# Optimization experiments

Hardware: AMD Instinct MI355X
Metric: run time of the kernel (lower is better)

The kernel has to match this reference:

```python
import jax, jax.numpy as jnp
import numpy as np

N_F, N_R = 50000, 25000
E_FF, E_RR, E_RF = 400000, 200000, 400000
D_N, D_F, D_R, D_E = 128, 128, 128, 64  # node-in, furn-out, room-out, edge dims
W_SCALE = 0.02


def _w(key, shape):
    # positive weights keep attention-score segment sums away from zero
    return jnp.abs(jax.random.normal(key, shape, dtype=jnp.float32)) * W_SCALE


def _edges(key, n_src, n_dst, n_edges):
    k1, k2 = jax.random.split(key)
    src = jax.random.randint(k1, (n_edges,), 0, n_src)
    # guarantee every dst node has >=1 in-edge of this etype
    dst = jnp.concatenate([jnp.arange(n_dst),
                           jax.random.randint(k2, (n_edges - n_dst,), 0, n_dst)])
    return src, dst


def setup_inputs() -> dict:
    key = jax.random.key(0)
    ks = jax.random.split(key, 24)
    ff_src, ff_dst = _edges(ks[0], N_F, N_F, E_FF)
    rr_src, rr_dst = _edges(ks[1], N_R, N_R, E_RR)
    rf_src, rf_dst = _edges(ks[2], N_R, N_F, E_RF)
    return {
        'f_feat': jax.random.uniform(ks[3], (N_F, D_N), dtype=jnp.float32),
        'r_feat': jax.random.uniform(ks[4], (N_R, D_N), dtype=jnp.float32),
        'ff_efeat': jax.random.uniform(ks[5], (E_FF, D_E), dtype=jnp.float32),
        'rr_efeat': jax.random.uniform(ks[6], (E_RR, D_E), dtype=jnp.float32),
        'rf_efeat': jax.random.uniform(ks[7], (E_RF, D_E), dtype=jnp.float32),
        # node / edge projections (nn.Linear weight stored transposed: [in, out])
        'Wf': _w(ks[8], (D_N, D_F)), 'Wr': _w(ks[9], (D_N, D_R)),
        'We_ff': _w(ks[10], (D_E, D_E)), 'We_rr': _w(ks[11], (D_E, D_E)), 'We_rf': _w(ks[12], (D_E, D_E)),
        # attention vectors (Linear(cat_dim, 1) flattened)
        'a_ff': _w(ks[13], (2 * D_F + D_E,)),
        'a_rr': _w(ks[14], (2 * D_R + D_E,)),
        'a_rf': _w(ks[15], (D_R + D_F + D_E,)),
        # node-out -> edge-out converters
        'Wec_ff': _w(ks[16], (D_F, D_E)), 'Wec_rr': _w(ks[17], (D_R, D_E)), 'Wec_rf': _w(ks[18], (D_F, D_E)),
        # edge-out -> node-out converters
        'Wnc_ff': _w(ks[19], (D_E, D_F)), 'Wnc_rr': _w(ks[20], (D_E, D_R)), 'Wnc_rf': _w(ks[21], (D_E, D_F)),
        'ff_src': ff_src, 'ff_dst': ff_dst,
        'rr_src': rr_src, 'rr_dst': rr_dst,
        'rf_src': rf_src, 'rf_dst': rf_dst,
    }


def _lrelu(x):
    return jnp.where(x >= 0, x, 0.01 * x)


def reference(f_feat, r_feat, ff_efeat, rr_efeat, rf_efeat,
              Wf, Wr, We_ff, We_rr, We_rf, a_ff, a_rr, a_rf,
              Wec_ff, Wec_rr, Wec_rf, Wnc_ff, Wnc_rr, Wnc_rf,
              ff_src, ff_dst, rr_src, rr_dst, rf_src, rf_dst):
    n_f, n_r = f_feat.shape[0], r_feat.shape[0]
    seg = jax.ops.segment_sum

    # node / edge linear projections (computed once per node/edge, then gathered)
    hf = f_feat @ Wf            # [N_F, D_F]
    hr = r_feat @ Wr            # [N_R, D_R]
    eff = ff_efeat @ We_ff      # [E_FF, D_E]
    err = rr_efeat @ We_rr
    erf = rf_efeat @ We_rf

    # attention scores: leakyrelu(a . [W_src(src), W_dst(dst), W_e(e)])
    # split a into per-slot vectors so per-node dots are computed once
    s_ff = _lrelu(jnp.take(hf @ a_ff[:D_F], ff_src) + jnp.take(hf @ a_ff[D_F:2 * D_F], ff_dst) + eff @ a_ff[2 * D_F:])
    s_rr = _lrelu(jnp.take(hr @ a_rr[:D_R], rr_src) + jnp.take(hr @ a_rr[D_R:2 * D_R], rr_dst) + err @ a_rr[2 * D_R:])
    s_rf = _lrelu(jnp.take(hr @ a_rf[:D_R], rf_src) + jnp.take(hf @ a_rf[D_R:D_R + D_F], rf_dst) + erf @ a_rf[D_R + D_F:])

    # sum_scores accumulated at DST nodes (DGL update_all over ff, rf, rr)
    sum_f = seg(s_ff, ff_dst, num_segments=n_f) + seg(s_rf, rf_dst, num_segments=n_f)
    sum_r = seg(s_rr, rr_dst, num_segments=n_r)

    # normalization divides by the SRC node's sum_scores (as in the source)
    s_ff = s_ff / jnp.take(sum_f, ff_src)
    s_rf = s_rf / jnp.take(sum_r, rf_src)
    s_rr = s_rr / jnp.take(sum_r, rr_src)

    # edge feature update: score * (W_e_convert(W_node(dst)) + W_e(e))
    new_eff = s_ff[:, None] * (jnp.take(hf @ Wec_ff, ff_dst, axis=0) + eff)
    new_err = s_rr[:, None] * (jnp.take(hr @ Wec_rr, rr_dst, axis=0) + err)
    new_erf = s_rf[:, None] * (jnp.take(hf @ Wec_rf, rf_dst, axis=0) + erf)

    # node updates: scatter-sum of W_node_convert(edge) to dst; matmul after sum
    upd_f = seg(new_eff, ff_dst, num_segments=n_f) @ Wnc_ff + seg(new_erf, rf_dst, num_segments=n_f) @ Wnc_rf
    upd_r = seg(new_err, rr_dst, num_segments=n_r) @ Wnc_rr

    new_f = hf + _lrelu(upd_f)
    new_r = hr + _lrelu(upd_r)
    return new_f, new_r, new_eff, new_err, new_erf
```

## Files before the change

kernel.cpp:

```cpp
#include <hip/hip_runtime.h>
#include <hip/hip_bf16.h>

#define LRELU(x) ((x) >= 0.f ? (x) : 0.01f * (x))

static constexpr int N_F = 50000, N_R = 25000;
static constexpr int E_FF = 400000, E_RR = 200000, E_RF = 400000;

static constexpr size_t OFF_NF  = 0;
static constexpr size_t OFF_NR  = OFF_NF + (size_t)N_F * 128;
static constexpr size_t OFF_EFF = OFF_NR + (size_t)N_R * 128;
static constexpr size_t OFF_ERR = OFF_EFF + (size_t)E_FF * 64;
static constexpr size_t OFF_ERF = OFF_ERR + (size_t)E_RR * 64;

static constexpr size_t WS_HF      = 0;
static constexpr size_t WS_HR      = WS_HF + (size_t)N_F * 128;
static constexpr size_t WS_GFC_FF  = WS_HR + (size_t)N_R * 128;
static constexpr size_t WS_GFC_RF  = WS_GFC_FF + (size_t)N_F * 64;
static constexpr size_t WS_GRC_RR  = WS_GFC_RF + (size_t)N_F * 64;
static constexpr size_t WS_DF_FFS  = WS_GRC_RR + (size_t)N_R * 64;
static constexpr size_t WS_DF_FFD  = WS_DF_FFS + N_F;
static constexpr size_t WS_DF_RFD  = WS_DF_FFD + N_F;
static constexpr size_t WS_DR_RRS  = WS_DF_RFD + N_F;
static constexpr size_t WS_DR_RRD  = WS_DR_RRS + N_R;
static constexpr size_t WS_DR_RFS  = WS_DR_RRD + N_R;
static constexpr size_t WS_SFF     = WS_DR_RFS + N_R;
static constexpr size_t WS_SRR     = WS_SFF + E_FF;
static constexpr size_t WS_SRF     = WS_SRR + E_RR;
static constexpr size_t WS_WT      = WS_SRF + E_RF;
static constexpr size_t WS_SUMF    = WS_WT + 192;
static constexpr size_t WS_SUMR    = WS_SUMF + N_F;
static constexpr size_t WS_AGGF    = WS_SUMR + N_R;
static constexpr size_t WS_AGGRR   = WS_AGGF + (size_t)N_F * 128;
static constexpr size_t WS_END     = WS_AGGRR + (size_t)N_R * 64;
static constexpr size_t ZERO_OFF   = WS_SUMF;
static constexpr size_t ZERO_CNT   = WS_END - WS_SUMF;

__global__ void wtilde_k(const float* __restrict__ We_ff, const float* __restrict__ We_rr,
                         const float* __restrict__ We_rf, const float* __restrict__ a_ff,
                         const float* __restrict__ a_rr, const float* __restrict__ a_rf,
                         float* __restrict__ wt) {
  int t = threadIdx.x;
  if (t >= 192) return;
  int grp = t >> 6, k = t & 63;
  const float* W = (grp == 0) ? We_ff : (grp == 1) ? We_rr : We_rf;
  const float* a = (grp == 0) ? a_ff + 256 : (grp == 1) ? a_rr + 256 : a_rf + 256;
  float s = 0.f;
  #pragma unroll 8
  for (int j = 0; j < 64; ++j) s += W[k * 64 + j] * a[j];
  wt[t] = s;
}

__global__ __launch_bounds__(256)
void gemm_dot3_128(const float* __restrict__ A, const float* __restrict__ W,
                   const float* __restrict__ a0, const float* __restrict__ a1,
                   const float* __restrict__ a2, float* __restrict__ C,
                   float* __restrict__ d0, float* __restrict__ d1,
                   float* __restrict__ d2, int M) {
  constexpr int K = 128, N = 128, BM = 64, BK = 32;
  __shared__ float As[BM][BK + 1];
  __shared__ float Ws[BK][N];
  const int t = threadIdx.x;
  const int row0 = (int)blockIdx.x * BM;
  const int rg = t >> 4, cg = t & 15;
  const int r0 = rg * 4, c0 = cg * 4;

  float acc[4][8];
  #pragma unroll
  for (int i = 0; i < 4; ++i)
    #pragma unroll
    for (int j = 0; j < 8; ++j) acc[i][j] = 0.f;

  for (int kb = 0; kb < K; kb += BK) {
    #pragma unroll
    for (int u = 0; u < 2; ++u) {
      int id = t + u * 256;
      int ar = id >> 3, ac = (id & 7) * 4;
      float4 v = make_float4(0.f, 0.f, 0.f, 0.f);
      int grow = row0 + ar;
      if (grow < M) v = *reinterpret_cast<const float4*>(&A[(size_t)grow * K + kb + ac]);
      As[ar][ac] = v.x; As[ar][ac + 1] = v.y; As[ar][ac + 2] = v.z; As[ar][ac + 3] = v.w;
    }
    #pragma unroll
    for (int u = 0; u < 4; ++u) {
      int id = t + u * 256;
      int wr = id >> 5, wc = (id & 31) * 4;
      *reinterpret_cast<float4*>(&Ws[wr][wc]) =
          *reinterpret_cast<const float4*>(&W[(size_t)(kb + wr) * N + wc]);
    }
    __syncthreads();
    #pragma unroll
    for (int k = 0; k < BK; ++k) {
      float av[4] = {As[r0][k], As[r0 + 1][k], As[r0 + 2][k], As[r0 + 3][k]};
      float4 w0 = *reinterpret_cast<const float4*>(&Ws[k][c0]);
      float4 w1 = *reinterpret_cast<const float4*>(&Ws[k][c0 + 64]);
      #pragma unroll
      for (int i = 0; i < 4; ++i) {
        acc[i][0] += av[i] * w0.x; acc[i][1] += av[i] * w0.y;
        acc[i][2] += av[i] * w0.z; acc[i][3] += av[i] * w0.w;
        acc[i][4] += av[i] * w1.x; acc[i][5] += av[i] * w1.y;
        acc[i][6] += av[i] * w1.z; acc[i][7] += av[i] * w1.w;
      }
    }
    __syncthreads();
  }
  float4 a0l = *reinterpret_cast<const float4*>(&a0[c0]);
  float4 a0h = *reinterpret_cast<const float4*>(&a0[c0 + 64]);
  float4 a1l = *reinterpret_cast<const float4*>(&a1[c0]);
  float4 a1h = *reinterpret_cast<const float4*>(&a1[c0 + 64]);
  float4 a2l = *reinterpret_cast<const float4*>(&a2[c0]);
  float4 a2h = *reinterpret_cast<const float4*>(&a2[c0 + 64]);
  #pragma unroll
  for (int i = 0; i < 4; ++i) {
    int grow = row0 + r0 + i;
    if (grow < M) {
      *reinterpret_cast<float4*>(&C[(size_t)grow * N + c0]) =
          make_float4(acc[i][0], acc[i][1], acc[i][2], acc[i][3]);
      *reinterpret_cast<float4*>(&C[(size_t)grow * N + c0 + 64]) =
          make_float4(acc[i][4], acc[i][5], acc[i][6], acc[i][7]);
    }
    float p0 = acc[i][0] * a0l.x + acc[i][1] * a0l.y + acc[i][2] * a0l.z + acc[i][3] * a0l.w
             + acc[i][4] * a0h.x + acc[i][5] * a0h.y + acc[i][6] * a0h.z + acc[i][7] * a0h.w;
    float p1 = acc[i][0] * a1l.x + acc[i][1] * a1l.y + acc[i][2] * a1l.z + acc[i][3] * a1l.w
             + acc[i][4] * a1h.x + acc[i][5] * a1h.y + acc[i][6] * a1h.z + acc[i][7] * a1h.w;
    float p2 = acc[i][0] * a2l.x + acc[i][1] * a2l.y + acc[i][2] * a2l.z + acc[i][3] * a2l.w
             + acc[i][4] * a2h.x + acc[i][5] * a2h.y + acc[i][6] * a2h.z + acc[i][7] * a2h.w;
    #pragma unroll
    for (int off = 1; off < 16; off <<= 1) {
      p0 += __shfl_xor(p0, off);
      p1 += __shfl_xor(p1, off);
      p2 += __shfl_xor(p2, off);
    }
    if (cg == 0 && grow < M) { d0[grow] = p0; d1[grow] = p1; d2[grow] = p2; }
  }
}

__global__ __launch_bounds__(256)
void gemm_128x64(const float* __restrict__ A, const float* __restrict__ W,
                 float* __restrict__ C, int M) {
  constexpr int K = 128, N = 64, BM = 64, BK = 32;
  __shared__ float As[BM][BK + 1];
  __shared__ float Ws[BK][N];
  const int t = threadIdx.x;
  const int row0 = (int)blockIdx.x * BM;
  const int rg = t >> 4, cg = t & 15;
  const int r0 = rg * 4, c0 = cg * 4;
  float acc[4][4];
  #pragma unroll
  for (int i = 0; i < 4; ++i)
    #pragma unroll
    for (int j = 0; j < 4; ++j) acc[i][j] = 0.f;

  for (int kb = 0; kb < K; kb += BK) {
    #pragma unroll
    for (int u = 0; u < 2; ++u) {
      int id = t + u * 256;
      int ar = id >> 3, ac = (id & 7) * 4;
      float4 v = make_float4(0.f, 0.f, 0.f, 0.f);
      int grow = row0 + ar;
      if (grow < M) v = *reinterpret_cast<const float4*>(&A[(size_t)grow * K + kb + ac]);
      As[ar][ac] = v.x; As[ar][ac + 1] = v.y; As[ar][ac + 2] = v.z; As[ar][ac + 3] = v.w;
    }
    #pragma unroll
    for (int u = 0; u < 2; ++u) {
      int id = t + u * 256;
      int wr = id >> 4, wc = (id & 15) * 4;
      *reinterpret_cast<float4*>(&Ws[wr][wc]) =
          *reinterpret_cast<const float4*>(&W[(size_t)(kb + wr) * N + wc]);
    }
    __syncthreads();
    #pragma unroll
    for (int k = 0; k < BK; ++k) {
      float av[4] = {As[r0][k], As[r0 + 1][k], As[r0 + 2][k], As[r0 + 3][k]};
      float4 w0 = *reinterpret_cast<const float4*>(&Ws[k][c0]);
      #pragma unroll
      for (int i = 0; i < 4; ++i) {
        acc[i][0] += av[i] * w0.x; acc[i][1] += av[i] * w0.y;
        acc[i][2] += av[i] * w0.z; acc[i][3] += av[i] * w0.w;
      }
    }
    __syncthreads();
  }
  #pragma unroll
  for (int i = 0; i < 4; ++i) {
    int grow = row0 + r0 + i;
    if (grow >= M) continue;
    *reinterpret_cast<float4*>(&C[(size_t)grow * N + c0]) =
        make_float4(acc[i][0], acc[i][1], acc[i][2], acc[i][3]);
  }
}

template<int K>
__global__ __launch_bounds__(256)
void node_update_k(const float* __restrict__ A, const float* __restrict__ W1,
                   const float* __restrict__ W2, const float* __restrict__ h,
                   float* __restrict__ C, int M) {
  constexpr int N = 128, BM = 64, BK = 32;
  __shared__ float As[BM][BK + 1];
  __shared__ float Ws[BK][N];
  const int t = threadIdx.x;
  const int row0 = (int)blockIdx.x * BM;
  const int rg = t >> 4, cg = t & 15;
  const int r0 = rg * 4, c0 = cg * 4;
  float acc[4][8];
  #pragma unroll
  for (int i = 0; i < 4; ++i)
    #pragma unroll
    for (int j = 0; j < 8; ++j) acc[i][j] = 0.f;

  for (int kb = 0; kb < K; kb += BK) {
    #pragma unroll
    for (int u = 0; u < 2; ++u) {
      int id = t + u * 256;
      int ar = id >> 3, ac = (id & 7) * 4;
      float4 v = make_float4(0.f, 0.f, 0.f, 0.f);
      int grow = row0 + ar;
      if (grow < M) v = *reinterpret_cast<const float4*>(&A[(size_t)grow * K + kb + ac]);
      As[ar][ac] = v.x; As[ar][ac + 1] = v.y; As[ar][ac + 2] = v.z; As[ar][ac + 3] = v.w;
    }
    #pragma unroll
    for (int u = 0; u < 4; ++u) {
      int id = t + u * 256;
      int wr = id >> 5, wc = (id & 31) * 4;
      int kr = kb + wr;
      const float* Wsrc = (K == 128 && kr >= 64) ? &W2[(size_t)(kr - 64) * N + wc]
                                                 : &W1[(size_t)kr * N + wc];
      *reinterpret_cast<float4*>(&Ws[wr][wc]) = *reinterpret_cast<const float4*>(Wsrc);
    }
    __syncthreads();
    #pragma unroll
    for (int k = 0; k < BK; ++k) {
      float av[4] = {As[r0][k], As[r0 + 1][k], As[r0 + 2][k], As[r0 + 3][k]};
      float4 w0 = *reinterpret_cast<const float4*>(&Ws[k][c0]);
      float4 w1 = *reinterpret_cast<const float4*>(&Ws[k][c0 + 64]);
      #pragma unroll
      for (int i = 0; i < 4; ++i) {
        acc[i][0] += av[i] * w0.x; acc[i][1] += av[i] * w0.y;
        acc[i][2] += av[i] * w0.z; acc[i][3] += av[i] * w0.w;
        acc[i][4] += av[i] * w1.x; acc[i][5] += av[i] * w1.y;
        acc[i][6] += av[i] * w1.z; acc[i][7] += av[i] * w1.w;
      }
    }
    __syncthreads();
  }
  #pragma unroll
  for (int i = 0; i < 4; ++i) {
    int grow = row0 + r0 + i;
    if (grow >= M) continue;
    float4 h0 = *reinterpret_cast<const float4*>(&h[(size_t)grow * N + c0]);
    float4 h1 = *reinterpret_cast<const float4*>(&h[(size_t)grow * N + c0 + 64]);
    float4 o0 = make_float4(h0.x + LRELU(acc[i][0]), h0.y + LRELU(acc[i][1]),
                            h0.z + LRELU(acc[i][2]), h0.w + LRELU(acc[i][3]));
    float4 o1 = make_float4(h1.x + LRELU(acc[i][4]), h1.y + LRELU(acc[i][5]),
                            h1.z + LRELU(acc[i][6]), h1.w + LRELU(acc[i][7]));
    *reinterpret_cast<float4*>(&C[(size_t)grow * N + c0]) = o0;
    *reinterpret_cast<float4*>(&C[(size_t)grow * N + c0 + 64]) = o1;
  }
}

__global__ __launch_bounds__(256)
void score_edge_k(const float* __restrict__ Ef, const float* __restrict__ wt,
                  const float* __restrict__ dsrc, const float* __restrict__ ddst,
                  const int* __restrict__ src, const int* __restrict__ dst,
                  float* __restrict__ s_out, float* __restrict__ sum_dst, int E) {
  int gid = (int)blockIdx.x * 256 + threadIdx.x;
  int e = gid >> 4;
  int l = gid & 15;
  if (e >= E) return;
  float4 ev = *reinterpret_cast<const float4*>(&Ef[(size_t)e * 64 + l * 4]);
  float4 av = *reinterpret_cast<const float4*>(&wt[l * 4]);
  float p = ev.x * av.x + ev.y * av.y + ev.z * av.z + ev.w * av.w;
  #pragma unroll
  for (int off = 1; off < 16; off <<= 1) p += __shfl_xor(p, off);
  if (l == 0) {
    float s = dsrc[src[e]] + ddst[dst[e]] + p;
    s = LRELU(s);
    s_out[e] = s;
    unsafeAtomicAdd(&sum_dst[dst[e]], s);
  }
}

__global__ __launch_bounds__(256)
void edge_proj_upd_k(const float* __restrict__ Ef, const float* __restrict__ W,
                     const float* __restrict__ g, const float* __restrict__ s_raw,
                     const float* __restrict__ sum_src, const int* __restrict__ src,
                     const int* __restrict__ dst, float* __restrict__ e_out,
                     float* __restrict__ agg, int agg_ld, int agg_off, int E) {
  constexpr int BM = 64, K = 64, N = 64;
  __shared__ float As[BM][K + 1];
  __shared__ float Ws[K][N];
  const int t = threadIdx.x;
  const int row0 = (int)blockIdx.x * BM;
  const int rg = t >> 4, cg = t & 15;
  const int r0 = rg * 4, c0 = cg * 4;

  #pragma unroll
  for (int u = 0; u < 4; ++u) {
    int id = t + u * 256;
    int ar = id >> 4, ac = (id & 15) * 4;
    float4 v = make_float4(0.f, 0.f, 0.f, 0.f);
    int ge = row0 + ar;
    if (ge < E) v = *reinterpret_cast<const float4*>(&Ef[(size_t)ge * K + ac]);
    As[ar][ac] = v.x; As[ar][ac + 1] = v.y; As[ar][ac + 2] = v.z; As[ar][ac + 3] = v.w;
  }
  #pragma unroll
  for (int u = 0; u < 4; ++u) {
    int id = t + u * 256;
    int wr = id >> 4, wc = (id & 15) * 4;
    *reinterpret_cast<float4*>(&Ws[wr][wc]) =
        *reinterpret_cast<const float4*>(&W[(size_t)wr * N + wc]);
  }
  __syncthreads();

  float acc[4][4];
  #pragma unroll
  for (int i = 0; i < 4; ++i)
    #pragma unroll
    for (int j = 0; j < 4; ++j) acc[i][j] = 0.f;
  #pragma unroll 8
  for (int k = 0; k < K; ++k) {
    float av[4] = {As[r0][k], As[r0 + 1][k], As[r0 + 2][k], As[r0 + 3][k]};
    float4 w0 = *reinterpret_cast<const float4*>(&Ws[k][c0]);
    #pragma unroll
    for (int i = 0; i < 4; ++i) {
      acc[i][0] += av[i] * w0.x; acc[i][1] += av[i] * w0.y;
      acc[i][2] += av[i] * w0.z; acc[i][3] += av[i] * w0.w;
    }
  }

  #pragma unroll
  for (int i = 0; i < 4; ++i) {
    int e = row0 + r0 + i;
    if (e >= E) continue;
    int d = dst[e];
    float s = s_raw[e] / sum_src[src[e]];
    float4 gv = *reinterpret_cast<const float4*>(&g[(size_t)d * 64 + c0]);
    float4 v = make_float4(s * (gv.x + acc[i][0]), s * (gv.y + acc[i][1]),
                           s * (gv.z + acc[i][2]), s * (gv.w + acc[i][3]));
    *reinterpret_cast<float4*>(&e_out[(size_t)e * 64 + c0]) = v;
    float* ap = &agg[(size_t)d * agg_ld + agg_off + c0];
    unsafeAtomicAdd(ap + 0, v.x);
    unsafeAtomicAdd(ap + 1, v.y);
    unsafeAtomicAdd(ap + 2, v.z);
    unsafeAtomicAdd(ap + 3, v.w);
  }
}

extern "C" void kernel_launch(void* const* d_in, const int* in_sizes, int n_in,
                              void* d_out, int out_size, void* d_ws, size_t ws_size,
                              hipStream_t stream) {
  const float* f_feat   = (const float*)d_in[0];
  const float* r_feat   = (const float*)d_in[1];
  const float* ff_efeat = (const float*)d_in[2];
  const float* rr_efeat = (const float*)d_in[3];
  const float* rf_efeat = (const float*)d_in[4];
  const float* Wf     = (const float*)d_in[5];
  const float* Wr     = (const float*)d_in[6];
  const float* We_ff  = (const float*)d_in[7];
  const float* We_rr  = (const float*)d_in[8];
  const float* We_rf  = (const float*)d_in[9];
  const float* a_ff   = (const float*)d_in[10];
  const float* a_rr   = (const float*)d_in[11];
  const float* a_rf   = (const float*)d_in[12];
  const float* Wec_ff = (const float*)d_in[13];
  const float* Wec_rr = (const float*)d_in[14];
  const float* Wec_rf = (const float*)d_in[15];
  const float* Wnc_ff = (const float*)d_in[16];
  const float* Wnc_rr = (const float*)d_in[17];
  const float* Wnc_rf = (const float*)d_in[18];
  const int* ff_src = (const int*)d_in[19];
  const int* ff_dst = (const int*)d_in[20];
  const int* rr_src = (const int*)d_in[21];
  const int* rr_dst = (const int*)d_in[22];
  const int* rf_src = (const int*)d_in[23];
  const int* rf_dst = (const int*)d_in[24];

  float* out = (float*)d_out;
  float* ws  = (float*)d_ws;

  float* hf     = ws + WS_HF;
  float* hr     = ws + WS_HR;
  float* gfc_ff = ws + WS_GFC_FF;
  float* gfc_rf = ws + WS_GFC_RF;
  float* grc_rr = ws + WS_GRC_RR;
  float* wt     = ws + WS_WT;
  float* sum_f  = ws + WS_SUMF;
  float* sum_r  = ws + WS_SUMR;
  float* agg_f  = ws + WS_AGGF;
  float* agg_rr = ws + WS_AGGRR;

  float* out_eff = out + OFF_EFF;
  float* out_err = out + OFF_ERR;
  float* out_erf = out + OFF_ERF;

  hipMemsetAsync(ws + ZERO_OFF, 0, ZERO_CNT * sizeof(float), stream);

  wtilde_k<<<1, 192, 0, stream>>>(We_ff, We_rr, We_rf, a_ff, a_rr, a_rf, wt);

  gemm_dot3_128<<<(N_F + 63) / 64, 256, 0, stream>>>(
      f_feat, Wf, a_ff, a_ff + 128, a_rf + 128, hf,
      ws + WS_DF_FFS, ws + WS_DF_FFD, ws + WS_DF_RFD, N_F);
  gemm_dot3_128<<<(N_R + 63) / 64, 256, 0, stream>>>(
      r_feat, Wr, a_rr, a_rr + 128, a_rf, hr,
      ws + WS_DR_RRS, ws + WS_DR_RRD, ws + WS_DR_RFS, N_R);

  gemm_128x64<<<(N_F + 63) / 64, 256, 0, stream>>>(hf, Wec_ff, gfc_ff, N_F);
  gemm_128x64<<<(N_F + 63) / 64, 256, 0, stream>>>(hf, Wec_rf, gfc_rf, N_F);
  gemm_128x64<<<(N_R + 63) / 64, 256, 0, stream>>>(hr, Wec_rr, grc_rr, N_R);

  score_edge_k<<<(E_FF * 16 + 255) / 256, 256, 0, stream>>>(
      ff_efeat, wt, ws + WS_DF_FFS, ws + WS_DF_FFD, ff_src, ff_dst,
      ws + WS_SFF, sum_f, E_FF);
  score_edge_k<<<(E_RR * 16 + 255) / 256, 256, 0, stream>>>(
      rr_efeat, wt + 64, ws + WS_DR_RRS, ws + WS_DR_RRD, rr_src, rr_dst,
      ws + WS_SRR, sum_r, E_RR);
  score_edge_k<<<(E_RF * 16 + 255) / 256, 256, 0, stream>>>(
      rf_efeat, wt + 128, ws + WS_DR_RFS, ws + WS_DF_RFD, rf_src, rf_dst,
      ws + WS_SRF, sum_f, E_RF);

  edge_proj_upd_k<<<(E_FF + 63) / 64, 256, 0, stream>>>(
      ff_efeat, We_ff, gfc_ff, ws + WS_SFF, sum_f, ff_src, ff_dst,
      out_eff, agg_f, 128, 0, E_FF);
  edge_proj_upd_k<<<(E_RR + 63) / 64, 256, 0, stream>>>(
      rr_efeat, We_rr, grc_rr, ws + WS_SRR, sum_r, rr_src, rr_dst,
      out_err, agg_rr, 64, 0, E_RR);
  edge_proj_upd_k<<<(E_RF + 63) / 64, 256, 0, stream>>>(
      rf_efeat, We_rf, gfc_rf, ws + WS_SRF, sum_r, rf_src, rf_dst,
      out_erf, agg_f, 128, 64, E_RF);

  node_update_k<128><<<(N_F + 63) / 64, 256, 0, stream>>>(
      agg_f, Wnc_ff, Wnc_rf, hf, out + OFF_NF, N_F);
  node_update_k<64><<<(N_R + 63) / 64, 256, 0, stream>>>(
      agg_rr, Wnc_rr, nullptr, hr, out + OFF_NR, N_R);
}
```

Baseline: 1.497 ms.

## Replace atomic scatter with CSR gather for score sums and node aggregation

Builds per-destination CSR edge lists each call (histogram, single-block scan, fill) and replaces the float atomicAdd scatters for score sums and edge-to-node aggregation with gather loops in dedicated kernels. Node update kernels now gather the edge outputs directly into shared memory before the matmul. The edge projection kernel uses a 128-row tile with a swizzled, transposed shared-memory layout. This removes the large aggregation memset and the atomic contention. The cost is extra CSR-building kernels, including serial single-block scans, and re-reading edge outputs through irregular gathers.

```diff
diff --git a/kernel.cpp b/kernel.cpp
--- a/kernel.cpp
+++ b/kernel.cpp
@@ -29,11 +29,18 @@
 static constexpr size_t WS_WT      = WS_SRF + E_RF;
 static constexpr size_t WS_SUMF    = WS_WT + 192;
 static constexpr size_t WS_SUMR    = WS_SUMF + N_F;
-static constexpr size_t WS_AGGF    = WS_SUMR + N_R;
-static constexpr size_t WS_AGGRR   = WS_AGGF + (size_t)N_F * 128;
-static constexpr size_t WS_END     = WS_AGGRR + (size_t)N_R * 64;
-static constexpr size_t ZERO_OFF   = WS_SUMF;
-static constexpr size_t ZERO_CNT   = WS_END - WS_SUMF;
+static constexpr size_t WS_INT     = WS_SUMR + N_R;
+
+static constexpr size_t I_CUR_FF = 0;
+static constexpr size_t I_CUR_RF = I_CUR_FF + N_F;
+static constexpr size_t I_CUR_RR = I_CUR_RF + N_F;
+static constexpr size_t I_ZERO_CNT = I_CUR_RR + N_R;
+static constexpr size_t I_OFF_FF = I_ZERO_CNT;
+static constexpr size_t I_OFF_RF = I_OFF_FF + N_F + 1;
+static constexpr size_t I_OFF_RR = I_OFF_RF + N_F + 1;
+static constexpr size_t I_EID_FF = I_OFF_RR + N_R + 1;
+static constexpr size_t I_EID_RF = I_EID_FF + E_FF;
+static constexpr size_t I_EID_RR = I_EID_RF + E_RF;
 
 __global__ void wtilde_k(const float* __restrict__ We_ff, const float* __restrict__ We_rr,
                          const float* __restrict__ We_rf, const float* __restrict__ a_ff,
@@ -51,6 +58,50 @@
 }
 
 __global__ __launch_bounds__(256)
+void hist_k(const int* __restrict__ dst, int* __restrict__ cnt, int E) {
+  int e = (int)blockIdx.x * 256 + threadIdx.x;
+  if (e < E) atomicAdd(&cnt[dst[e]], 1);
+}
+
+__global__ __launch_bounds__(1024)
+void scan_k(int* __restrict__ cnt ,
+            int* __restrict__ off , int n) {
+  __shared__ int ls[1024];
+  int t = threadIdx.x;
+  int chunk = (n + 1023) / 1024;
+  int beg = t * chunk;
+  int end = beg + chunk < n ? beg + chunk : n;
+  int s = 0;
+  for (int i = beg; i < end; ++i) s += cnt[i];
+  ls[t] = s;
+  __syncthreads();
+  for (int d = 1; d < 1024; d <<= 1) {
+    int v = (t >= d) ? ls[t - d] : 0;
+    __syncthreads();
+    ls[t] += v;
+    __syncthreads();
+  }
+  int run = (t == 0) ? 0 : ls[t - 1];
+  for (int i = beg; i < end; ++i) {
+    int c = cnt[i];
+    off[i] = run;
+    cnt[i] = run;
+    run += c;
+  }
+  if (t == 1023) off[n] = ls[1023];
+}
+
+__global__ __launch_bounds__(256)
+void fill_k(const int* __restrict__ dst, int* __restrict__ cur,
+            int* __restrict__ eid, int E) {
+  int e = (int)blockIdx.x * 256 + threadIdx.x;
+  if (e < E) {
+    int pos = atomicAdd(&cur[dst[e]], 1);
+    eid[pos] = e;
+  }
+}
+
+__global__ __launch_bounds__(256)
 void gemm_dot3_128(const float* __restrict__ A, const float* __restrict__ W,
                    const float* __restrict__ a0, const float* __restrict__ a1,
                    const float* __restrict__ a2, float* __restrict__ C,
@@ -189,16 +240,145 @@
   }
 }
 
-template<int K>
-__global__ __launch_bounds__(256)
-void node_update_k(const float* __restrict__ A, const float* __restrict__ W1,
-                   const float* __restrict__ W2, const float* __restrict__ h,
-                   float* __restrict__ C, int M) {
-  constexpr int N = 128, BM = 64, BK = 32;
-  __shared__ float As[BM][BK + 1];
+__global__ __launch_bounds__(256)
+void score_edge_k(const float* __restrict__ Ef, const float* __restrict__ wt,
+                  const float* __restrict__ dsrc, const float* __restrict__ ddst,
+                  const int* __restrict__ src, const int* __restrict__ dst,
+                  float* __restrict__ s_out, int E) {
+  int gid = (int)blockIdx.x * 256 + threadIdx.x;
+  int e = gid >> 4;
+  int l = gid & 15;
+  if (e >= E) return;
+  float4 ev = *reinterpret_cast<const float4*>(&Ef[(size_t)e * 64 + l * 4]);
+  float4 av = *reinterpret_cast<const float4*>(&wt[l * 4]);
+  float p = ev.x * av.x + ev.y * av.y + ev.z * av.z + ev.w * av.w;
+  #pragma unroll
+  for (int off = 1; off < 16; off <<= 1) p += __shfl_xor(p, off);
+  if (l == 0) {
+    float s = dsrc[src[e]] + ddst[dst[e]] + p;
+    s_out[e] = LRELU(s);
+  }
+}
+
+__global__ __launch_bounds__(256)
+void sum_csr_k(const int* __restrict__ offA, const int* __restrict__ eidA,
+               const float* __restrict__ sA,
+               const int* __restrict__ offB, const int* __restrict__ eidB,
+               const float* __restrict__ sB,
+               float* __restrict__ sum, int n) {
+  int d = (int)blockIdx.x * 256 + threadIdx.x;
+  if (d >= n) return;
+  float s = 0.f;
+  int b = offA[d], e = offA[d + 1];
+  for (int j = b; j < e; ++j) s += sA[eidA[j]];
+  if (offB) {
+    b = offB[d]; e = offB[d + 1];
+    for (int j = b; j < e; ++j) s += sB[eidB[j]];
+  }
+  sum[d] = s;
+}
+
+__global__ __launch_bounds__(256)
+void edge_proj_upd_k(const float* __restrict__ Ef, const float* __restrict__ W,
+                     const float* __restrict__ g, const float* __restrict__ s_raw,
+                     const float* __restrict__ sum_src, const int* __restrict__ src,
+                     const int* __restrict__ dst, float* __restrict__ e_out, int E) {
+  constexpr int BM = 128, K = 64, N = 64;
+  __shared__ float AsT[K][BM];
+  __shared__ float Ws[K][N];
+  const int t = threadIdx.x;
+  const int row0 = (int)blockIdx.x * BM;
+  const int rg = t >> 4, cg = t & 15;
+  const int r0 = rg * 8, c0 = cg * 4;
+
+  #pragma unroll
+  for (int u = 0; u < 8; ++u) {
+    int id = t + u * 256;
+    int ar = id >> 4;
+    int ac = (id & 15) * 4;
+    float4 v = make_float4(0.f, 0.f, 0.f, 0.f);
+    int ge = row0 + ar;
+    if (ge < E) v = *reinterpret_cast<const float4*>(&Ef[(size_t)ge * K + ac]);
+    int glo = ar & 3, gr = ar >> 2;
+    AsT[ac + 0][((gr ^ (((ac + 0) >> 2) & 7)) << 2) | glo] = v.x;
+    AsT[ac + 1][((gr ^ (((ac + 1) >> 2) & 7)) << 2) | glo] = v.y;
+    AsT[ac + 2][((gr ^ (((ac + 2) >> 2) & 7)) << 2) | glo] = v.z;
+    AsT[ac + 3][((gr ^ (((ac + 3) >> 2) & 7)) << 2) | glo] = v.w;
+  }
+  #pragma unroll
+  for (int u = 0; u < 4; ++u) {
+    int id = t + u * 256;
+    int wr = id >> 4, wc = (id & 15) * 4;
+    *reinterpret_cast<float4*>(&Ws[wr][wc]) =
+        *reinterpret_cast<const float4*>(&W[(size_t)wr * N + wc]);
+  }
+  __syncthreads();
+
+  float acc[8][4];
+  #pragma unroll
+  for (int i = 0; i < 8; ++i)
+    #pragma unroll
+    for (int j = 0; j < 4; ++j) acc[i][j] = 0.f;
+
+  const int gb = r0 >> 2;
+  for (int k4 = 0; k4 < 16; ++k4) {
+    int s = k4 & 7;
+    int ca = (gb ^ s) << 2;
+    int cb = ((gb + 1) ^ s) << 2;
+    #pragma unroll
+    for (int j4 = 0; j4 < 4; ++j4) {
+      int k = k4 * 4 + j4;
+      float4 a0 = *reinterpret_cast<const float4*>(&AsT[k][ca]);
+      float4 a1 = *reinterpret_cast<const float4*>(&AsT[k][cb]);
+      float4 w  = *reinterpret_cast<const float4*>(&Ws[k][c0]);
+      #pragma unroll
+      for (int j = 0; j < 4; ++j) {
+        float wj = (&w.x)[j];
+        acc[0][j] += a0.x * wj; acc[1][j] += a0.y * wj;
+        acc[2][j] += a0.z * wj; acc[3][j] += a0.w * wj;
+        acc[4][j] += a1.x * wj; acc[5][j] += a1.y * wj;
+        acc[6][j] += a1.z * wj; acc[7][j] += a1.w * wj;
+      }
+    }
+  }
+
+  #pragma unroll
+  for (int i = 0; i < 8; ++i) {
+    int e = row0 + r0 + i;
+    if (e >= E) continue;
+    int d = dst[e];
+    float s = s_raw[e] / sum_src[src[e]];
+    float4 gv = *reinterpret_cast<const float4*>(&g[(size_t)d * 64 + c0]);
+    float4 v = make_float4(s * (gv.x + acc[i][0]), s * (gv.y + acc[i][1]),
+                           s * (gv.z + acc[i][2]), s * (gv.w + acc[i][3]));
+    *reinterpret_cast<float4*>(&e_out[(size_t)e * 64 + c0]) = v;
+  }
+}
+
+__global__ __launch_bounds__(256)
+void node_upd_f_k(const float* __restrict__ e_ff, const float* __restrict__ e_rf,
+                  const int* __restrict__ off_ff, const int* __restrict__ eid_ff,
+                  const int* __restrict__ off_rf, const int* __restrict__ eid_rf,
+                  const float* __restrict__ W1, const float* __restrict__ W2,
+                  const float* __restrict__ h, float* __restrict__ C, int M) {
+  constexpr int BM = 64, K = 128, N = 128, BK = 32;
+  __shared__ float As[BM][K + 1];
   __shared__ float Ws[BK][N];
   const int t = threadIdx.x;
   const int row0 = (int)blockIdx.x * BM;
+  const int wv = t >> 6, l = t & 63;
+  for (int r = wv; r < BM; r += 4) {
+    int d = row0 + r;
+    float a0 = 0.f, a1 = 0.f;
+    if (d < M) {
+      int b = off_ff[d], e2 = off_ff[d + 1];
+      for (int j = b; j < e2; ++j) a0 += e_ff[(size_t)eid_ff[j] * 64 + l];
+      b = off_rf[d]; e2 = off_rf[d + 1];
+      for (int j = b; j < e2; ++j) a1 += e_rf[(size_t)eid_rf[j] * 64 + l];
+    }
+    As[r][l] = a0;
+    As[r][l + 64] = a1;
+  }
   const int rg = t >> 4, cg = t & 15;
   const int r0 = rg * 4, c0 = cg * 4;
   float acc[4][8];
@@ -208,28 +388,21 @@
     for (int j = 0; j < 8; ++j) acc[i][j] = 0.f;
 
   for (int kb = 0; kb < K; kb += BK) {
-    #pragma unroll
-    for (int u = 0; u < 2; ++u) {
-      int id = t + u * 256;
-      int ar = id >> 3, ac = (id & 7) * 4;
-      float4 v = make_float4(0.f, 0.f, 0.f, 0.f);
-      int grow = row0 + ar;
-      if (grow < M) v = *reinterpret_cast<const float4*>(&A[(size_t)grow * K + kb + ac]);
-      As[ar][ac] = v.x; As[ar][ac + 1] = v.y; As[ar][ac + 2] = v.z; As[ar][ac + 3] = v.w;
-    }
+    __syncthreads();
     #pragma unroll
     for (int u = 0; u < 4; ++u) {
       int id = t + u * 256;
       int wr = id >> 5, wc = (id & 31) * 4;
       int kr = kb + wr;
-      const float* Wsrc = (K == 128 && kr >= 64) ? &W2[(size_t)(kr - 64) * N + wc]
-                                                 : &W1[(size_t)kr * N + wc];
+      const float* Wsrc = (kr >= 64) ? &W2[(size_t)(kr - 64) * N + wc]
+                                     : &W1[(size_t)kr * N + wc];
       *reinterpret_cast<float4*>(&Ws[wr][wc]) = *reinterpret_cast<const float4*>(Wsrc);
     }
     __syncthreads();
     #pragma unroll
     for (int k = 0; k < BK; ++k) {
-      float av[4] = {As[r0][k], As[r0 + 1][k], As[r0 + 2][k], As[r0 + 3][k]};
+      int kk = kb + k;
+      float av[4] = {As[r0][kk], As[r0 + 1][kk], As[r0 + 2][kk], As[r0 + 3][kk]};
       float4 w0 = *reinterpret_cast<const float4*>(&Ws[k][c0]);
       float4 w1 = *reinterpret_cast<const float4*>(&Ws[k][c0 + 64]);
       #pragma unroll
@@ -240,7 +413,6 @@
         acc[i][6] += av[i] * w1.z; acc[i][7] += av[i] * w1.w;
       }
     }
-    __syncthreads();
   }
   #pragma unroll
   for (int i = 0; i < 4; ++i) {
@@ -258,90 +430,71 @@
 }
 
 __global__ __launch_bounds__(256)
-void score_edge_k(const float* __restrict__ Ef, const float* __restrict__ wt,
-                  const float* __restrict__ dsrc, const float* __restrict__ ddst,
-                  const int* __restrict__ src, const int* __restrict__ dst,
-                  float* __restrict__ s_out, float* __restrict__ sum_dst, int E) {
-  int gid = (int)blockIdx.x * 256 + threadIdx.x;
-  int e = gid >> 4;
-  int l = gid & 15;
-  if (e >= E) return;
-  float4 ev = *reinterpret_cast<const float4*>(&Ef[(size_t)e * 64 + l * 4]);
-  float4 av = *reinterpret_cast<const float4*>(&wt[l * 4]);
-  float p = ev.x * av.x + ev.y * av.y + ev.z * av.z + ev.w * av.w;
-  #pragma unroll
-  for (int off = 1; off < 16; off <<= 1) p += __shfl_xor(p, off);
-  if (l == 0) {
-    float s = dsrc[src[e]] + ddst[dst[e]] + p;
-    s = LRELU(s);
-    s_out[e] = s;
-    unsafeAtomicAdd(&sum_dst[dst[e]], s);
-  }
-}
-
-__global__ __launch_bounds__(256)
-void edge_proj_upd_k(const float* __restrict__ Ef, const float* __restrict__ W,
-                     const float* __restrict__ g, const float* __restrict__ s_raw,
-                     const float* __restrict__ sum_src, const int* __restrict__ src,
-                     const int* __restrict__ dst, float* __restrict__ e_out,
-                     float* __restrict__ agg, int agg_ld, int agg_off, int E) {
-  constexpr int BM = 64, K = 64, N = 64;
+void node_upd_r_k(const float* __restrict__ e_rr,
+                  const int* __restrict__ off_rr, const int* __restrict__ eid_rr,
+                  const float* __restrict__ W1, const float* __restrict__ h,
+                  float* __restrict__ C, int M) {
+  constexpr int BM = 64, K = 64, N = 128, BK = 32;
   __shared__ float As[BM][K + 1];
-  __shared__ float Ws[K][N];
+  __shared__ float Ws[BK][N];
   const int t = threadIdx.x;
   const int row0 = (int)blockIdx.x * BM;
+  const int wv = t >> 6, l = t & 63;
+  for (int r = wv; r < BM; r += 4) {
+    int d = row0 + r;
+    float a0 = 0.f;
+    if (d < M) {
+      int b = off_rr[d], e2 = off_rr[d + 1];
+      for (int j = b; j < e2; ++j) a0 += e_rr[(size_t)eid_rr[j] * 64 + l];
+    }
+    As[r][l] = a0;
+  }
   const int rg = t >> 4, cg = t & 15;
   const int r0 = rg * 4, c0 = cg * 4;
-
-  #pragma unroll
-  for (int u = 0; u < 4; ++u) {
-    int id = t + u * 256;
-    int ar = id >> 4, ac = (id & 15) * 4;
-    float4 v = make_float4(0.f, 0.f, 0.f, 0.f);
-    int ge = row0 + ar;
-    if (ge < E) v = *reinterpret_cast<const float4*>(&Ef[(size_t)ge * K + ac]);
-    As[ar][ac] = v.x; As[ar][ac + 1] = v.y; As[ar][ac + 2] = v.z; As[ar][ac + 3] = v.w;
-  }
-  #pragma unroll
-  for (int u = 0; u < 4; ++u) {
-    int id = t + u * 256;
-    int wr = id >> 4, wc = (id & 15) * 4;
-    *reinterpret_cast<float4*>(&Ws[wr][wc]) =
-        *reinterpret_cast<const float4*>(&W[(size_t)wr * N + wc]);
-  }
-  __syncthreads();
-
-  float acc[4][4];
+  float acc[4][8];
   #pragma unroll
   for (int i = 0; i < 4; ++i)
     #pragma unroll
-    for (int j = 0; j < 4; ++j) acc[i][j] = 0.f;
-  #pragma unroll 8
-  for (int k = 0; k < K; ++k) {
-    float av[4] = {As[r0][k], As[r0 + 1][k], As[r0 + 2][k], As[r0 + 3][k]};
-    float4 w0 = *reinterpret_cast<const float4*>(&Ws[k][c0]);
-    #pragma unroll
-    for (int i = 0; i < 4; ++i) {
-      acc[i][0] += av[i] * w0.x; acc[i][1] += av[i] * w0.y;
-      acc[i][2] += av[i] * w0.z; acc[i][3] += av[i] * w0.w;
-    }
-  }
-
+    for (int j = 0; j < 8; ++j) acc[i][j] = 0.f;
+
+  for (int kb = 0; kb < K; kb += BK) {
+    __syncthreads();
+    #pragma unroll
+    for (int u = 0; u < 4; ++u) {
+      int id = t + u * 256;
+      int wr = id >> 5, wc = (id & 31) * 4;
+      int kr = kb + wr;
+      *reinterpret_cast<float4*>(&Ws[wr][wc]) =
+          *reinterpret_cast<const float4*>(&W1[(size_t)kr * N + wc]);
+    }
+    __syncthreads();
+    #pragma unroll
+    for (int k = 0; k < BK; ++k) {
+      int kk = kb + k;
+      float av[4] = {As[r0][kk], As[r0 + 1][kk], As[r0 + 2][kk], As[r0 + 3][kk]};
+      float4 w0 = *reinterpret_cast<const float4*>(&Ws[k][c0]);
+      float4 w1 = *reinterpret_cast<const float4*>(&Ws[k][c0 + 64]);
+      #pragma unroll
+      for (int i = 0; i < 4; ++i) {
+        acc[i][0] += av[i] * w0.x; acc[i][1] += av[i] * w0.y;
+        acc[i][2] += av[i] * w0.z; acc[i][3] += av[i] * w0.w;
+        acc[i][4] += av[i] * w1.x; acc[i][5] += av[i] * w1.y;
+        acc[i][6] += av[i] * w1.z; acc[i][7] += av[i] * w1.w;
+      }
+    }
+  }
   #pragma unroll
   for (int i = 0; i < 4; ++i) {
-    int e = row0 + r0 + i;
-    if (e >= E) continue;
-    int d = dst[e];
-    float s = s_raw[e] / sum_src[src[e]];
-    float4 gv = *reinterpret_cast<const float4*>(&g[(size_t)d * 64 + c0]);
-    float4 v = make_float4(s * (gv.x + acc[i][0]), s * (gv.y + acc[i][1]),
-                           s * (gv.z + acc[i][2]), s * (gv.w + acc[i][3]));
-    *reinterpret_cast<float4*>(&e_out[(size_t)e * 64 + c0]) = v;
-    float* ap = &agg[(size_t)d * agg_ld + agg_off + c0];
-    unsafeAtomicAdd(ap + 0, v.x);
-    unsafeAtomicAdd(ap + 1, v.y);
-    unsafeAtomicAdd(ap + 2, v.z);
-    unsafeAtomicAdd(ap + 3, v.w);
+    int grow = row0 + r0 + i;
+    if (grow >= M) continue;
+    float4 h0 = *reinterpret_cast<const float4*>(&h[(size_t)grow * N + c0]);
+    float4 h1 = *reinterpret_cast<const float4*>(&h[(size_t)grow * N + c0 + 64]);
+    float4 o0 = make_float4(h0.x + LRELU(acc[i][0]), h0.y + LRELU(acc[i][1]),
+                            h0.z + LRELU(acc[i][2]), h0.w + LRELU(acc[i][3]));
+    float4 o1 = make_float4(h1.x + LRELU(acc[i][4]), h1.y + LRELU(acc[i][5]),
+                            h1.z + LRELU(acc[i][6]), h1.w + LRELU(acc[i][7]));
+    *reinterpret_cast<float4*>(&C[(size_t)grow * N + c0]) = o0;
+    *reinterpret_cast<float4*>(&C[(size_t)grow * N + c0 + 64]) = o1;
   }
 }
 
@@ -376,6 +529,7 @@
 
   float* out = (float*)d_out;
   float* ws  = (float*)d_ws;
+  int*   wsI = (int*)(ws + WS_INT);
 
   float* hf     = ws + WS_HF;
   float* hr     = ws + WS_HR;
@@ -385,16 +539,34 @@
   float* wt     = ws + WS_WT;
   float* sum_f  = ws + WS_SUMF;
   float* sum_r  = ws + WS_SUMR;
-  float* agg_f  = ws + WS_AGGF;
-  float* agg_rr = ws + WS_AGGRR;
+
+  int* cur_ff = wsI + I_CUR_FF;
+  int* cur_rf = wsI + I_CUR_RF;
+  int* cur_rr = wsI + I_CUR_RR;
+  int* off_ff = wsI + I_OFF_FF;
+  int* off_rf = wsI + I_OFF_RF;
+  int* off_rr = wsI + I_OFF_RR;
+  int* eid_ff = wsI + I_EID_FF;
+  int* eid_rf = wsI + I_EID_RF;
+  int* eid_rr = wsI + I_EID_RR;
 
   float* out_eff = out + OFF_EFF;
   float* out_err = out + OFF_ERR;
   float* out_erf = out + OFF_ERF;
 
-  hipMemsetAsync(ws + ZERO_OFF, 0, ZERO_CNT * sizeof(float), stream);
+  hipMemsetAsync(wsI, 0, I_ZERO_CNT * sizeof(int), stream);
 
   wtilde_k<<<1, 192, 0, stream>>>(We_ff, We_rr, We_rf, a_ff, a_rr, a_rf, wt);
+
+  hist_k<<<(E_FF + 255) / 256, 256, 0, stream>>>(ff_dst, cur_ff, E_FF);
+  hist_k<<<(E_RF + 255) / 256, 256, 0, stream>>>(rf_dst, cur_rf, E_RF);
+  hist_k<<<(E_RR + 255) / 256, 256, 0, stream>>>(rr_dst, cur_rr, E_RR);
+  scan_k<<<1, 1024, 0, stream>>>(cur_ff, off_ff, N_F);
+  scan_k<<<1, 1024, 0, stream>>>(cur_rf, off_rf, N_F);
+  scan_k<<<1, 1024, 0, stream>>>(cur_rr, off_rr, N_R);
+  fill_k<<<(E_FF + 255) / 256, 256, 0, stream>>>(ff_dst, cur_ff, eid_ff, E_FF);
+  fill_k<<<(E_RF + 255) / 256, 256, 0, stream>>>(rf_dst, cur_rf, eid_rf, E_RF);
+  fill_k<<<(E_RR + 255) / 256, 256, 0, stream>>>(rr_dst, cur_rr, eid_rr, E_RR);
 
   gemm_dot3_128<<<(N_F + 63) / 64, 256, 0, stream>>>(
       f_feat, Wf, a_ff, a_ff + 128, a_rf + 128, hf,
@@ -409,26 +581,29 @@
 
   score_edge_k<<<(E_FF * 16 + 255) / 256, 256, 0, stream>>>(
       ff_efeat, wt, ws + WS_DF_FFS, ws + WS_DF_FFD, ff_src, ff_dst,
-      ws + WS_SFF, sum_f, E_FF);
+      ws + WS_SFF, E_FF);
   score_edge_k<<<(E_RR * 16 + 255) / 256, 256, 0, stream>>>(
       rr_efeat, wt + 64, ws + WS_DR_RRS, ws + WS_DR_RRD, rr_src, rr_dst,
-      ws + WS_SRR, sum_r, E_RR);
+      ws + WS_SRR, E_RR);
   score_edge_k<<<(E_RF * 16 + 255) / 256, 256, 0, stream>>>(
       rf_efeat, wt + 128, ws + WS_DR_RFS, ws + WS_DF_RFD, rf_src, rf_dst,
-      ws + WS_SRF, sum_f, E_RF);
-
-  edge_proj_upd_k<<<(E_FF + 63) / 64, 256, 0, stream>>>(
-      ff_efeat, We_ff, gfc_ff, ws + WS_SFF, sum_f, ff_src, ff_dst,
-      out_eff, agg_f, 128, 0, E_FF);
-  edge_proj_upd_k<<<(E_RR + 63) / 64, 256, 0, stream>>>(
-      rr_efeat, We_rr, grc_rr, ws + WS_SRR, sum_r, rr_src, rr_dst,
-      out_err, agg_rr, 64, 0, E_RR);
-  edge_proj_upd_k<<<(E_RF + 63) / 64, 256, 0, stream>>>(
-      rf_efeat, We_rf, gfc_rf, ws + WS_SRF, sum_r, rf_src, rf_dst,
-      out_erf, agg_f, 128, 64, E_RF);
-
-  node_update_k<128><<<(N_F + 63) / 64, 256, 0, stream>>>(
-      agg_f, Wnc_ff, Wnc_rf, hf, out + OFF_NF, N_F);
-  node_update_k<64><<<(N_R + 63) / 64, 256, 0, stream>>>(
-      agg_rr, Wnc_rr, nullptr, hr, out + OFF_NR, N_R);
-}
+      ws + WS_SRF, E_RF);
+
+  sum_csr_k<<<(N_F + 255) / 256, 256, 0, stream>>>(
+      off_ff, eid_ff, ws + WS_SFF, off_rf, eid_rf, ws + WS_SRF, sum_f, N_F);
+  sum_csr_k<<<(N_R + 255) / 256, 256, 0, stream>>>(
+      off_rr, eid_rr, ws + WS_SRR, nullptr, nullptr, nullptr, sum_r, N_R);
+
+  edge_proj_upd_k<<<(E_FF + 127) / 128, 256, 0, stream>>>(
+      ff_efeat, We_ff, gfc_ff, ws + WS_SFF, sum_f, ff_src, ff_dst, out_eff, E_FF);
+  edge_proj_upd_k<<<(E_RR + 127) / 128, 256, 0, stream>>>(
+      rr_efeat, We_rr, grc_rr, ws + WS_SRR, sum_r, rr_src, rr_dst, out_err, E_RR);
+  edge_proj_upd_k<<<(E_RF + 127) / 128, 256, 0, stream>>>(
+      rf_efeat, We_rf, gfc_rf, ws + WS_SRF, sum_r, rf_src, rf_dst, out_erf, E_RF);
+
+  node_upd_f_k<<<(N_F + 63) / 64, 256, 0, stream>>>(
+      out_eff, out_erf, off_ff, eid_ff, off_rf, eid_rf,
+      Wnc_ff, Wnc_rf, hf, out + OFF_NF, N_F);
+  node_upd_r_k<<<(N_R + 63) / 64, 256, 0, stream>>>(
+      out_err, off_rr, eid_rr, Wnc_rr, hr, out + OFF_NR, N_R);
+}
```

Result: slower. 1.745 ms (+16.6%).
